# Performance work log

Measured on AMD Instinct MI355X. Metric: run time of the kernel, lower is better.

Reference implementation:

```python
import jax, jax.numpy as jnp
import numpy as np

N_NODES = 20000
N_EDGES = 120000
N_GRAPHS = 512
F_IN = 300
NHID = 256
NHID_FF = 256
NOUT = 768
SLOPE = 0.2
EPS = 1e-16


def _p(key, shape, scale=0.05):
    return jax.random.normal(key, shape, dtype=jnp.float32) * scale


def setup_inputs() -> dict:
    key = jax.random.key(0)
    ks = jax.random.split(key, 24)
    inp = {
        "x": jax.random.normal(ks[0], (N_NODES, F_IN), dtype=jnp.float32),
        "edge_index": jax.random.randint(ks[1], (2, N_EDGES), 0, N_NODES, dtype=jnp.int64) if False else jax.random.randint(ks[1], (2, N_EDGES), 0, N_NODES).astype(jnp.int32),
        "batch": jnp.sort(jax.random.randint(ks[2], (N_NODES,), 0, N_GRAPHS)).astype(jnp.int32),
        # conv1: in=300 -> heads=4, C=256, concat
        "c1_wl": _p(ks[3], (4 * NHID, F_IN)),
        "c1_wr": _p(ks[4], (4 * NHID, F_IN)),
        "c1_att": _p(ks[5], (4, NHID)),
        "c1_b": jnp.zeros((4 * NHID,), jnp.float32),
        # conv2: in=1024 -> heads=4, C=256, concat
        "c2_wl": _p(ks[6], (4 * NHID, 4 * NHID)),
        "c2_wr": _p(ks[7], (4 * NHID, 4 * NHID)),
        "c2_att": _p(ks[8], (4, NHID)),
        "c2_b": jnp.zeros((4 * NHID,), jnp.float32),
        # conv3: in=1024 -> heads=6, C=256, mean (concat=False)
        "c3_wl": _p(ks[9], (6 * NHID_FF, 4 * NHID)),
        "c3_wr": _p(ks[10], (6 * NHID_FF, 4 * NHID)),
        "c3_att": _p(ks[11], (6, NHID_FF)),
        "c3_b": jnp.zeros((NHID_FF,), jnp.float32),
        # post-process MLP
        "fp1_w": _p(ks[12], (NHID_FF, NHID_FF)),
        "fp1_b": jnp.zeros((NHID_FF,), jnp.float32),
        "fp2_w": _p(ks[13], (NOUT, NHID_FF)),
        "fp2_b": jnp.zeros((NOUT,), jnp.float32),
    }
    return inp


def gatv2(x, src, dst, wl, wr, att, b, concat):
    """GATv2Conv (PyG semantics, eval mode): lin_l on source, lin_r on target,
    score = att . leaky_relu(xl_j + xr_i), segment softmax over dst, aggregate xl_j."""
    n = x.shape[0]
    H, C = att.shape
    xl = (x @ wl.T).reshape(n, H, C)
    xr = (x @ wr.T).reshape(n, H, C)
    s = xl[src] + xr[dst]                                   # [E,H,C] gather
    s = jnp.where(s > 0, s, SLOPE * s)                      # leaky_relu
    scores = jnp.einsum("ehc,hc->eh", s, att)               # [E,H]
    mx = jax.ops.segment_max(scores, dst, num_segments=n)   # [N,H]
    ex = jnp.exp(scores - mx[dst])
    denom = jax.ops.segment_sum(ex, dst, num_segments=n)
    alpha = ex / (denom[dst] + EPS)                         # [E,H]
    out = jax.ops.segment_sum(alpha[:, :, None] * xl[src], dst, num_segments=n)  # [N,H,C]
    out = out.reshape(n, H * C) if concat else out.mean(axis=1)
    return out + b


def reference(x, edge_index, batch, c1_wl, c1_wr, c1_att, c1_b,
              c2_wl, c2_wr, c2_att, c2_b, c3_wl, c3_wr, c3_att, c3_b,
              fp1_w, fp1_b, fp2_w, fp2_b):
    n = x.shape[0]
    # PyG GATv2Conv defaults add_self_loops=True
    loops = jnp.arange(n, dtype=edge_index.dtype)
    src = jnp.concatenate([edge_index[0], loops])
    dst = jnp.concatenate([edge_index[1], loops])

    h = jax.nn.elu(gatv2(x, src, dst, c1_wl, c1_wr, c1_att, c1_b, concat=True))
    h = jax.nn.elu(gatv2(h, src, dst, c2_wl, c2_wr, c2_att, c2_b, concat=True))
    h = gatv2(h, src, dst, c3_wl, c3_wr, c3_att, c3_b, concat=False)

    # F.normalize(p=2, dim=-1), torch eps=1e-12
    norm = jnp.linalg.norm(h, axis=-1, keepdims=True)
    h = h / jnp.maximum(norm, 1e-12)

    # global_mean_pool over `batch`
    sums = jax.ops.segment_sum(h, batch, num_segments=N_GRAPHS)
    cnts = jax.ops.segment_sum(jnp.ones((n,), h.dtype), batch, num_segments=N_GRAPHS)
    pooled = sums / jnp.maximum(cnts, 1.0)[:, None]

    h = jax.nn.relu(pooled @ fp1_w.T + fp1_b)
    return h @ fp2_w.T + fp2_b
```

## Files before the change

kernel.cpp:

```cpp
#include <hip/hip_runtime.h>

typedef _Float16 h16;
typedef _Float16 h16x2 __attribute__((ext_vector_type(2)));
typedef _Float16 h16x4 __attribute__((ext_vector_type(4)));
typedef _Float16 h16x8 __attribute__((ext_vector_type(8)));
typedef float f32x4 __attribute__((ext_vector_type(4)));

static constexpr int NN   = 20000;
static constexpr int NPAD = 20224;
static constexpr int NE0  = 120000;
static constexpr int NE   = 140000;
static constexpr int NG   = 512;
static constexpr int FIN  = 300;
static constexpr int K1P  = 384;
static constexpr int CD   = 256;
static constexpr float SLOPE = 0.2f;

#define GLDS16(gsrc, ldst)                                                              \
  __builtin_amdgcn_global_load_lds(                                                    \
      (const __attribute__((address_space(1))) unsigned int*)(gsrc),                    \
      (__attribute__((address_space(3))) unsigned int*)(ldst), 16, 0, 0)

#define MFMA16(a, b, c) __builtin_amdgcn_mfma_f32_16x16x32_f16(a, b, c, 0, 0, 0)

__global__ __launch_bounds__(256) void fill_x_kernel(const float* __restrict__ x, h16* __restrict__ a1) {
  int r = blockIdx.x;
  for (int c = threadIdx.x; c < K1P; c += 256) {
    float v = (r < NN && c < FIN) ? x[(size_t)r * FIN + c] : 0.f;
    a1[(size_t)r * K1P + c] = (h16)v;
  }
}

__global__ __launch_bounds__(256) void conv_w2_kernel(const float* __restrict__ wl, const float* __restrict__ wr,
                                                      h16* __restrict__ o, int rows, int cols, int colsp) {
  int r = blockIdx.x;
  const float* s = (r < rows) ? (wl + (size_t)r * cols) : (wr + (size_t)(r - rows) * cols);
  for (int c = threadIdx.x; c < colsp; c += 256) {
    float v = (c < cols) ? s[c] : 0.f;
    o[(size_t)r * colsp + c] = (h16)v;
  }
}

__global__ __launch_bounds__(256) void attcvt_kernel(const float* __restrict__ a, h16* __restrict__ o, int n) {
  int i = blockIdx.x * 256 + threadIdx.x;
  if (i < n) o[i] = (h16)a[i];
}

__global__ __launch_bounds__(256) void build_edges_kernel(const int* __restrict__ ei,
                                                          int* __restrict__ src, int* __restrict__ dst) {
  int e = blockIdx.x * 256 + threadIdx.x;
  if (e >= NE) return;
  if (e < NE0) { src[e] = ei[e]; dst[e] = ei[NE0 + e]; }
  else         { src[e] = e - NE0; dst[e] = e - NE0; }
}

__global__ __launch_bounds__(256) void deg_kernel(const int* __restrict__ dst, int* __restrict__ deg) {
  int e = blockIdx.x * 256 + threadIdx.x;
  if (e < NE) atomicAdd(&deg[dst[e]], 1);
}

__global__ __launch_bounds__(1024) void scan_kernel(const int* __restrict__ deg, int* __restrict__ rowptr) {
  __shared__ int b0[1024], b1[1024];
  __shared__ int carry;
  int t = threadIdx.x;
  if (t == 0) carry = 0;
  __syncthreads();
  for (int base = 0; base < NN; base += 1024) {
    int x = (base + t < NN) ? deg[base + t] : 0;
    b0[t] = x;
    __syncthreads();
    int* cur = b0; int* nxt = b1;
    for (int off = 1; off < 1024; off <<= 1) {
      int v = cur[t];
      if (t >= off) v += cur[t - off];
      nxt[t] = v;
      __syncthreads();
      int* tmp = cur; cur = nxt; nxt = tmp;
    }
    if (base + t < NN) rowptr[base + t] = carry + cur[t] - x;
    __syncthreads();
    if (t == 0) carry += cur[1023];
    __syncthreads();
  }
  if (t == 0) rowptr[NN] = carry;
}

__global__ __launch_bounds__(256) void scatter_kernel(const int* __restrict__ src, const int* __restrict__ dst,
                                                      const int* __restrict__ rowptr, int* __restrict__ cursor,
                                                      int* __restrict__ esrc) {
  int e = blockIdx.x * 256 + threadIdx.x;
  if (e >= NE) return;
  int d = dst[e];
  int pos = rowptr[d] + atomicAdd(&cursor[d], 1);
  esrc[pos] = src[e];
}

__global__ __launch_bounds__(512, 2) void gemm256_kernel(const h16* __restrict__ A, const h16* __restrict__ B,
                                                         h16* __restrict__ Co, int K, int Nw, int ntN) {
  __shared__ __align__(16) h16 lds[4 * 16384];
  int nwg = gridDim.x;
  int q = nwg >> 3, r = nwg & 7;
  int xc = blockIdx.x & 7, idx = blockIdx.x >> 3;
  int logical = (xc < r ? xc * (q + 1) : r * (q + 1) + (xc - r) * q) + idx;
  int tm = (logical / ntN) * 256, tn = (logical % ntN) * 256;

  int tid = threadIdx.x;
  int wv = tid >> 6, lane = tid & 63;
  int wm = (wv >> 2) * 128, wn = (wv & 3) * 64;
  int lrow = lane & 15, kq = lane >> 4, lr7 = lrow & 7;

  int rowoff = tid >> 3;
  int ug = ((tid & 7) ^ (rowoff & 7)) * 8;
  int ldsoff = (tid >> 6) * 512;

  const int NT = K >> 6;

  auto STAGE = [&](int buf, int kt) {
#pragma unroll
    for (int j = 0; j < 4; ++j) {
      GLDS16(A + (size_t)(tm + j * 64 + rowoff) * K + kt * 64 + ug,
             &lds[(buf * 2 + 0) * 16384 + j * 4096 + ldsoff]);
      GLDS16(B + (size_t)(tn + j * 64 + rowoff) * K + kt * 64 + ug,
             &lds[(buf * 2 + 1) * 16384 + j * 4096 + ldsoff]);
    }
  };

  STAGE(0, 0);
  STAGE(1, 1);

  f32x4 acc[8][4] = {};
  for (int t = 0; t < NT; ++t) {
    int b = t & 1;
    if (t + 1 < NT) { asm volatile("s_waitcnt vmcnt(8)" ::: "memory"); }
    else            { asm volatile("s_waitcnt vmcnt(0)" ::: "memory"); }
    __builtin_amdgcn_s_barrier();

    const h16* As_ = &lds[(b * 2 + 0) * 16384];
    const h16* Bs_ = &lds[(b * 2 + 1) * 16384];
    int u0 = (kq ^ lr7) * 8;
    int u1 = ((4 + kq) ^ lr7) * 8;
    h16x8 af[8], bf[4];

#pragma unroll
    for (int i = 0; i < 8; ++i) af[i] = *(const h16x8*)&As_[(wm + i * 16 + lrow) * 64 + u0];
    bf[0] = *(const h16x8*)&Bs_[(wn + 0 * 16 + lrow) * 64 + u0];
    bf[1] = *(const h16x8*)&Bs_[(wn + 1 * 16 + lrow) * 64 + u0];
    __builtin_amdgcn_s_setprio(1);
#pragma unroll
    for (int i = 0; i < 8; ++i) {
      acc[i][0] = MFMA16(af[i], bf[0], acc[i][0]);
      acc[i][1] = MFMA16(af[i], bf[1], acc[i][1]);
    }
    __builtin_amdgcn_s_setprio(0);
    __builtin_amdgcn_sched_barrier(0);

    bf[2] = *(const h16x8*)&Bs_[(wn + 2 * 16 + lrow) * 64 + u0];
    bf[3] = *(const h16x8*)&Bs_[(wn + 3 * 16 + lrow) * 64 + u0];
    __builtin_amdgcn_s_setprio(1);
#pragma unroll
    for (int i = 0; i < 8; ++i) {
      acc[i][2] = MFMA16(af[i], bf[2], acc[i][2]);
      acc[i][3] = MFMA16(af[i], bf[3], acc[i][3]);
    }
    __builtin_amdgcn_s_setprio(0);
    __builtin_amdgcn_sched_barrier(0);

#pragma unroll
    for (int i = 0; i < 8; ++i) af[i] = *(const h16x8*)&As_[(wm + i * 16 + lrow) * 64 + u1];
    bf[0] = *(const h16x8*)&Bs_[(wn + 0 * 16 + lrow) * 64 + u1];
    bf[1] = *(const h16x8*)&Bs_[(wn + 1 * 16 + lrow) * 64 + u1];
    __builtin_amdgcn_s_setprio(1);
#pragma unroll
    for (int i = 0; i < 8; ++i) {
      acc[i][0] = MFMA16(af[i], bf[0], acc[i][0]);
      acc[i][1] = MFMA16(af[i], bf[1], acc[i][1]);
    }
    __builtin_amdgcn_s_setprio(0);
    __builtin_amdgcn_sched_barrier(0);

    bf[2] = *(const h16x8*)&Bs_[(wn + 2 * 16 + lrow) * 64 + u1];
    bf[3] = *(const h16x8*)&Bs_[(wn + 3 * 16 + lrow) * 64 + u1];
    asm volatile("s_waitcnt lgkmcnt(0)" ::: "memory");
    __builtin_amdgcn_sched_barrier(0);
    __builtin_amdgcn_s_barrier();
    if (t + 2 < NT) STAGE(b, t + 2);
    __builtin_amdgcn_s_setprio(1);
#pragma unroll
    for (int i = 0; i < 8; ++i) {
      acc[i][2] = MFMA16(af[i], bf[2], acc[i][2]);
      acc[i][3] = MFMA16(af[i], bf[3], acc[i][3]);
    }
    __builtin_amdgcn_s_setprio(0);
  }

  int cr = kq * 4, cc = lrow;
#pragma unroll
  for (int i = 0; i < 8; ++i)
#pragma unroll
    for (int j = 0; j < 4; ++j) {
      size_t base = (size_t)(tm + wm + i * 16 + cr) * Nw + (tn + wn + j * 16 + cc);
#pragma unroll
      for (int qq = 0; qq < 4; qq++) Co[base + (size_t)qq * Nw] = (h16)acc[i][j][qq];
    }
}

template <int H, int MODE>
__global__ __launch_bounds__(64 * H) void sagg_kernel(
    const h16* __restrict__ X, const int* __restrict__ rowptr, const int* __restrict__ esrc,
    const h16* __restrict__ attH, const float* __restrict__ bias,
    h16* __restrict__ outA, const int* __restrict__ batch,
    float* __restrict__ pooled, int* __restrict__ cnt) {
  constexpr int HC = H * CD, S = 2 * HC;
  int n = blockIdx.x;
  int tid = threadIdx.x, w = tid >> 6, lane = tid & 63;
  int cb = w * CD + lane * 4;

  h16x4 aw4 = *(const h16x4*)(attH + cb);
  h16x2 alo = __builtin_shufflevector(aw4, aw4, 0, 1);
  h16x2 ahi = __builtin_shufflevector(aw4, aw4, 2, 3);
  h16x4 xr4 = *(const h16x4*)(X + (size_t)n * S + HC + cb);

  int beg = rowptr[n], end = rowptr[n + 1];
  float m = -1e30f, s = 0.f;
  f32x4 a = {};
  int i = beg;
  while (i < end) {
    int cn = end - i; if (cn > 8) cn = 8;
    int js[8];
    h16x4 xs[8];
    float ps[8];
#pragma unroll
    for (int k = 0; k < 8; ++k) js[k] = esrc[i + (k < cn ? k : cn - 1)];
#pragma unroll
    for (int k = 0; k < 8; ++k) xs[k] = *(const h16x4*)(X + (size_t)js[k] * S + cb);
#pragma unroll
    for (int k = 0; k < 8; ++k) {
      h16x4 v = xs[k] + xr4;
      h16x4 t = v * (h16)SLOPE;
      v = __builtin_elementwise_max(v, t);
      float p = __builtin_amdgcn_fdot2(__builtin_shufflevector(v, v, 0, 1), alo,
                __builtin_amdgcn_fdot2(__builtin_shufflevector(v, v, 2, 3), ahi, 0.f, false), false);
      p += __shfl_xor(p, 32); p += __shfl_xor(p, 16); p += __shfl_xor(p, 8);
      p += __shfl_xor(p, 4);  p += __shfl_xor(p, 2);  p += __shfl_xor(p, 1);
      ps[k] = p;
    }
#pragma unroll
    for (int k = 0; k < 8; ++k) {
      if (k < cn) {
        float p = ps[k];
        if (p <= m) {
          float we = __expf(p - m);
          s += we;
          a[0] += we * (float)xs[k][0]; a[1] += we * (float)xs[k][1];
          a[2] += we * (float)xs[k][2]; a[3] += we * (float)xs[k][3];
        } else {
          float f = __expf(m - p);
          s = s * f + 1.f;
          a[0] = a[0] * f + (float)xs[k][0]; a[1] = a[1] * f + (float)xs[k][1];
          a[2] = a[2] * f + (float)xs[k][2]; a[3] = a[3] * f + (float)xs[k][3];
          m = p;
        }
      }
    }
    i += cn;
  }
  float inv = 1.f / (s + 1e-16f);

  if (MODE == 0) {
    float o0 = a[0] * inv + bias[cb + 0];
    float o1 = a[1] * inv + bias[cb + 1];
    float o2 = a[2] * inv + bias[cb + 2];
    float o3 = a[3] * inv + bias[cb + 3];
    o0 = o0 > 0.f ? o0 : expm1f(o0);
    o1 = o1 > 0.f ? o1 : expm1f(o1);
    o2 = o2 > 0.f ? o2 : expm1f(o2);
    o3 = o3 > 0.f ? o3 : expm1f(o3);
    h16x4 ov = {(h16)o0, (h16)o1, (h16)o2, (h16)o3};
    *(h16x4*)(outA + (size_t)n * HC + cb) = ov;
  } else {
    __shared__ float sh[HC];
    __shared__ float red[H];
    float4 nv = {a[0] * inv, a[1] * inv, a[2] * inv, a[3] * inv};
    *(float4*)&sh[cb] = nv;
    __syncthreads();
    float mv = 0.f;
    if (tid < CD) {
#pragma unroll
      for (int h = 0; h < H; h++) mv += sh[h * CD + tid];
      mv = mv * (1.f / H) + bias[tid];
    }
    float ss = (tid < CD) ? mv * mv : 0.f;
    ss += __shfl_xor(ss, 32); ss += __shfl_xor(ss, 16); ss += __shfl_xor(ss, 8);
    ss += __shfl_xor(ss, 4);  ss += __shfl_xor(ss, 2);  ss += __shfl_xor(ss, 1);
    if (lane == 0) red[w] = ss;
    __syncthreads();
    float tot = 0.f;
#pragma unroll
    for (int h = 0; h < H; h++) tot += red[h];
    float scale = 1.f / fmaxf(sqrtf(tot), 1e-12f);
    int g = batch[n];
    if (tid < CD) atomicAdd(&pooled[(size_t)g * CD + tid], mv * scale);
    if (tid == 0) atomicAdd(&cnt[g], 1);
  }
}

__global__ __launch_bounds__(256) void pool_div_kernel(float* __restrict__ pooled, const int* __restrict__ cnt) {
  int g = blockIdx.x, t = threadIdx.x;
  pooled[(size_t)g * CD + t] /= fmaxf((float)cnt[g], 1.f);
}

__global__ __launch_bounds__(256) void mlp1_kernel(const float* __restrict__ pooled, const float* __restrict__ w,
                                                   const float* __restrict__ b, float* __restrict__ hid) {
  __shared__ float xs[CD];
  int g = blockIdx.x, t = threadIdx.x;
  xs[t] = pooled[(size_t)g * CD + t];
  __syncthreads();
  float acc = b[t];
  for (int k = 0; k < CD; ++k) acc += xs[k] * w[(size_t)t * CD + k];
  hid[(size_t)g * CD + t] = fmaxf(acc, 0.f);
}

__global__ __launch_bounds__(256) void mlp2_kernel(const float* __restrict__ hid, const float* __restrict__ w,
                                                   const float* __restrict__ b, float* __restrict__ out) {
  __shared__ float xs[CD];
  int g = blockIdx.x, t = threadIdx.x;
  xs[t] = hid[(size_t)g * CD + t];
  __syncthreads();
  for (int o = t; o < 768; o += 256) {
    float acc = b[o];
    for (int k = 0; k < CD; ++k) acc += xs[k] * w[(size_t)o * CD + k];
    out[(size_t)g * 768 + o] = acc;
  }
}

extern "C" void kernel_launch(void* const* d_in, const int* in_sizes, int n_in,
                              void* d_out, int out_size, void* d_ws, size_t ws_size,
                              hipStream_t stream) {
  const float* x      = (const float*)d_in[0];
  const int*   ei     = (const int*)d_in[1];
  const int*   batch  = (const int*)d_in[2];
  const float* c1_wl  = (const float*)d_in[3];
  const float* c1_wr  = (const float*)d_in[4];
  const float* c1_att = (const float*)d_in[5];
  const float* c1_b   = (const float*)d_in[6];
  const float* c2_wl  = (const float*)d_in[7];
  const float* c2_wr  = (const float*)d_in[8];
  const float* c2_att = (const float*)d_in[9];
  const float* c2_b   = (const float*)d_in[10];
  const float* c3_wl  = (const float*)d_in[11];
  const float* c3_wr  = (const float*)d_in[12];
  const float* c3_att = (const float*)d_in[13];
  const float* c3_b   = (const float*)d_in[14];
  const float* fp1_w  = (const float*)d_in[15];
  const float* fp1_b  = (const float*)d_in[16];
  const float* fp2_w  = (const float*)d_in[17];
  const float* fp2_b  = (const float*)d_in[18];

  char* p = (char*)d_ws;
  size_t off = 0;
  auto alloc = [&](size_t b) { void* r = p + off; off += (b + 255) & ~(size_t)255; return r; };
  h16*  A    = (h16*)alloc((size_t)NPAD * 1024 * 2);
  h16*  Xa   = (h16*)alloc((size_t)NPAD * 3072 * 2);
  h16*  Xb   = (h16*)alloc((size_t)NPAD * 2048 * 2);
  h16*  A1   = Xb;
  h16*  W1   = (h16*)alloc((size_t)2048 * K1P * 2);
  h16*  W2   = (h16*)alloc((size_t)2048 * 1024 * 2);
  h16*  W3   = (h16*)alloc((size_t)3072 * 1024 * 2);
  h16*  attH1 = (h16*)alloc((size_t)4 * CD * 2);
  h16*  attH2 = (h16*)alloc((size_t)4 * CD * 2);
  h16*  attH3 = (h16*)alloc((size_t)6 * CD * 2);
  int*  srcA   = (int*)alloc((size_t)NE * 4);
  int*  dstA   = (int*)alloc((size_t)NE * 4);
  int*  esrc   = (int*)alloc((size_t)NE * 4);
  int*  deg    = (int*)alloc((size_t)NN * 4);
  int*  cursor = (int*)alloc((size_t)NN * 4);
  int*  rowptr = (int*)alloc((size_t)(NN + 1) * 4);
  float* pooled = (float*)alloc((size_t)NG * CD * 4);
  int*  cnt    = (int*)alloc((size_t)NG * 4);
  float* hid   = (float*)alloc((size_t)NG * CD * 4);

  hipMemsetAsync(deg, 0, (size_t)NN * 4, stream);
  hipMemsetAsync(cursor, 0, (size_t)NN * 4, stream);
  hipMemsetAsync(pooled, 0, (size_t)NG * CD * 4, stream);
  hipMemsetAsync(cnt, 0, (size_t)NG * 4, stream);

  fill_x_kernel<<<NPAD, 256, 0, stream>>>(x, A1);
  conv_w2_kernel<<<2048, 256, 0, stream>>>(c1_wl, c1_wr, W1, 1024, FIN, K1P);
  conv_w2_kernel<<<2048, 256, 0, stream>>>(c2_wl, c2_wr, W2, 1024, 1024, 1024);
  conv_w2_kernel<<<3072, 256, 0, stream>>>(c3_wl, c3_wr, W3, 1536, 1024, 1024);
  attcvt_kernel<<<4, 256, 0, stream>>>(c1_att, attH1, 4 * CD);
  attcvt_kernel<<<4, 256, 0, stream>>>(c2_att, attH2, 4 * CD);
  attcvt_kernel<<<6, 256, 0, stream>>>(c3_att, attH3, 6 * CD);

  int eb = (NE + 255) / 256;
  build_edges_kernel<<<eb, 256, 0, stream>>>(ei, srcA, dstA);
  deg_kernel<<<eb, 256, 0, stream>>>(dstA, deg);
  scan_kernel<<<1, 1024, 0, stream>>>(deg, rowptr);
  scatter_kernel<<<eb, 256, 0, stream>>>(srcA, dstA, rowptr, cursor, esrc);

  gemm256_kernel<<<79 * 8, 512, 0, stream>>>(A1, W1, Xa, K1P, 2048, 8);
  sagg_kernel<4, 0><<<NN, 256, 0, stream>>>(Xa, rowptr, esrc, attH1, c1_b, A, nullptr, nullptr, nullptr);

  gemm256_kernel<<<79 * 8, 512, 0, stream>>>(A, W2, Xb, 1024, 2048, 8);
  sagg_kernel<4, 0><<<NN, 256, 0, stream>>>(Xb, rowptr, esrc, attH2, c2_b, A, nullptr, nullptr, nullptr);

  gemm256_kernel<<<79 * 12, 512, 0, stream>>>(A, W3, Xa, 1024, 3072, 12);
  sagg_kernel<6, 1><<<NN, 384, 0, stream>>>(Xa, rowptr, esrc, attH3, c3_b, nullptr, batch, pooled, cnt);

  pool_div_kernel<<<NG, 256, 0, stream>>>(pooled, cnt);
  mlp1_kernel<<<NG, 256, 0, stream>>>(pooled, fp1_w, fp1_b, hid);
  mlp2_kernel<<<NG, 256, 0, stream>>>(hid, fp2_w, fp2_b, (float*)d_out);
}
```

Measured before the change: 695.0 us.

## Load full k-tile fragments up front and interleave global-to-LDS staging with MFMA

```diff
diff --git a/kernel.cpp b/kernel.cpp
--- a/kernel.cpp
+++ b/kernel.cpp
@@ -115,18 +115,17 @@
 
   const int NT = K >> 6;
 
-  auto STAGE = [&](int buf, int kt) {
-#pragma unroll
-    for (int j = 0; j < 4; ++j) {
-      GLDS16(A + (size_t)(tm + j * 64 + rowoff) * K + kt * 64 + ug,
-             &lds[(buf * 2 + 0) * 16384 + j * 4096 + ldsoff]);
-      GLDS16(B + (size_t)(tn + j * 64 + rowoff) * K + kt * 64 + ug,
-             &lds[(buf * 2 + 1) * 16384 + j * 4096 + ldsoff]);
-    }
+  auto STAGE1 = [&](int buf, int kt, int j) {
+    GLDS16(A + (size_t)(tm + j * 64 + rowoff) * K + kt * 64 + ug,
+           &lds[(buf * 2 + 0) * 16384 + j * 4096 + ldsoff]);
+    GLDS16(B + (size_t)(tn + j * 64 + rowoff) * K + kt * 64 + ug,
+           &lds[(buf * 2 + 1) * 16384 + j * 4096 + ldsoff]);
   };
 
-  STAGE(0, 0);
-  STAGE(1, 1);
+#pragma unroll
+  for (int j = 0; j < 4; ++j) STAGE1(0, 0, j);
+#pragma unroll
+  for (int j = 0; j < 4; ++j) STAGE1(1, 1, j);
 
   f32x4 acc[8][4] = {};
   for (int t = 0; t < NT; ++t) {
@@ -139,56 +138,54 @@
     const h16* Bs_ = &lds[(b * 2 + 1) * 16384];
     int u0 = (kq ^ lr7) * 8;
     int u1 = ((4 + kq) ^ lr7) * 8;
-    h16x8 af[8], bf[4];
-
-#pragma unroll
-    for (int i = 0; i < 8; ++i) af[i] = *(const h16x8*)&As_[(wm + i * 16 + lrow) * 64 + u0];
-    bf[0] = *(const h16x8*)&Bs_[(wn + 0 * 16 + lrow) * 64 + u0];
-    bf[1] = *(const h16x8*)&Bs_[(wn + 1 * 16 + lrow) * 64 + u0];
-    __builtin_amdgcn_s_setprio(1);
-#pragma unroll
-    for (int i = 0; i < 8; ++i) {
-      acc[i][0] = MFMA16(af[i], bf[0], acc[i][0]);
-      acc[i][1] = MFMA16(af[i], bf[1], acc[i][1]);
-    }
-    __builtin_amdgcn_s_setprio(0);
-    __builtin_amdgcn_sched_barrier(0);
-
-    bf[2] = *(const h16x8*)&Bs_[(wn + 2 * 16 + lrow) * 64 + u0];
-    bf[3] = *(const h16x8*)&Bs_[(wn + 3 * 16 + lrow) * 64 + u0];
-    __builtin_amdgcn_s_setprio(1);
-#pragma unroll
-    for (int i = 0; i < 8; ++i) {
-      acc[i][2] = MFMA16(af[i], bf[2], acc[i][2]);
-      acc[i][3] = MFMA16(af[i], bf[3], acc[i][3]);
-    }
-    __builtin_amdgcn_s_setprio(0);
-    __builtin_amdgcn_sched_barrier(0);
-
-#pragma unroll
-    for (int i = 0; i < 8; ++i) af[i] = *(const h16x8*)&As_[(wm + i * 16 + lrow) * 64 + u1];
-    bf[0] = *(const h16x8*)&Bs_[(wn + 0 * 16 + lrow) * 64 + u1];
-    bf[1] = *(const h16x8*)&Bs_[(wn + 1 * 16 + lrow) * 64 + u1];
-    __builtin_amdgcn_s_setprio(1);
-#pragma unroll
-    for (int i = 0; i < 8; ++i) {
-      acc[i][0] = MFMA16(af[i], bf[0], acc[i][0]);
-      acc[i][1] = MFMA16(af[i], bf[1], acc[i][1]);
-    }
-    __builtin_amdgcn_s_setprio(0);
-    __builtin_amdgcn_sched_barrier(0);
-
-    bf[2] = *(const h16x8*)&Bs_[(wn + 2 * 16 + lrow) * 64 + u1];
-    bf[3] = *(const h16x8*)&Bs_[(wn + 3 * 16 + lrow) * 64 + u1];
+
+    h16x8 af0[8], bf0[4], af1[8], bf1[4];
+#pragma unroll
+    for (int i = 0; i < 8; ++i) af0[i] = *(const h16x8*)&As_[(wm + i * 16 + lrow) * 64 + u0];
+#pragma unroll
+    for (int j = 0; j < 4; ++j) bf0[j] = *(const h16x8*)&Bs_[(wn + j * 16 + lrow) * 64 + u0];
+#pragma unroll
+    for (int i = 0; i < 8; ++i) af1[i] = *(const h16x8*)&As_[(wm + i * 16 + lrow) * 64 + u1];
+#pragma unroll
+    for (int j = 0; j < 4; ++j) bf1[j] = *(const h16x8*)&Bs_[(wn + j * 16 + lrow) * 64 + u1];
     asm volatile("s_waitcnt lgkmcnt(0)" ::: "memory");
     __builtin_amdgcn_sched_barrier(0);
     __builtin_amdgcn_s_barrier();
-    if (t + 2 < NT) STAGE(b, t + 2);
+
+    bool st = (t + 2 < NT);
+    if (st) STAGE1(b, t + 2, 0);
     __builtin_amdgcn_s_setprio(1);
 #pragma unroll
     for (int i = 0; i < 8; ++i) {
-      acc[i][2] = MFMA16(af[i], bf[2], acc[i][2]);
-      acc[i][3] = MFMA16(af[i], bf[3], acc[i][3]);
+      acc[i][0] = MFMA16(af0[i], bf0[0], acc[i][0]);
+      acc[i][1] = MFMA16(af0[i], bf0[1], acc[i][1]);
+    }
+    __builtin_amdgcn_s_setprio(0);
+    __builtin_amdgcn_sched_barrier(0);
+    if (st) STAGE1(b, t + 2, 1);
+    __builtin_amdgcn_s_setprio(1);
+#pragma unroll
+    for (int i = 0; i < 8; ++i) {
+      acc[i][2] = MFMA16(af0[i], bf0[2], acc[i][2]);
+      acc[i][3] = MFMA16(af0[i], bf0[3], acc[i][3]);
+    }
+    __builtin_amdgcn_s_setprio(0);
+    __builtin_amdgcn_sched_barrier(0);
+    if (st) STAGE1(b, t + 2, 2);
+    __builtin_amdgcn_s_setprio(1);
+#pragma unroll
+    for (int i = 0; i < 8; ++i) {
+      acc[i][0] = MFMA16(af1[i], bf1[0], acc[i][0]);
+      acc[i][1] = MFMA16(af1[i], bf1[1], acc[i][1]);
+    }
+    __builtin_amdgcn_s_setprio(0);
+    __builtin_amdgcn_sched_barrier(0);
+    if (st) STAGE1(b, t + 2, 3);
+    __builtin_amdgcn_s_setprio(1);
+#pragma unroll
+    for (int i = 0; i < 8; ++i) {
+      acc[i][2] = MFMA16(af1[i], bf1[2], acc[i][2]);
+      acc[i][3] = MFMA16(af1[i], bf1[3], acc[i][3]);
     }
     __builtin_amdgcn_s_setprio(0);
   }
```

Result: no change. 700.6 us (+0.8%).
